# Kernel tuning notes

Hardware: AMD Instinct MI355X
Metric: run time of the kernel (lower is better)

The kernel has to match this reference:

```python
import jax, jax.numpy as jnp
import numpy as np


def setup_inputs() -> dict:
    key = jax.random.key(0)
    ks = jax.random.split(key, 7)
    bs, win_len, num_obj, d = 4, 64, 36, 2048
    s = 1.0 / np.sqrt(d)
    return {
        "region_feats": jax.random.normal(ks[0], (bs, win_len, num_obj, d), jnp.float32),
        "Wq": jax.random.normal(ks[1], (d, d), jnp.float32) * s,
        "bq": jax.random.normal(ks[2], (d,), jnp.float32) * 0.01,
        "Wk": jax.random.normal(ks[3], (d, d), jnp.float32) * s,
        "bk": jax.random.normal(ks[4], (d,), jnp.float32) * 0.01,
        "Wu": jax.random.normal(ks[5], (d, 1024), jnp.float32) * s,
        "bu": jax.random.normal(ks[6], (1024,), jnp.float32) * 0.01,
    }


def reference(region_feats, Wq, bq, Wk, bk, Wu, bu):
    bs, win_len, num_obj, d = region_feats.shape
    feats = region_feats.reshape(bs, win_len * num_obj, d)  # [b, n, d]
    q = feats @ Wq + bq                                     # [b, n, d]
    k = feats @ Wk + bk                                     # [b, n, d]
    adj = jnp.einsum('bnd,bmd->bnm', q, k)                  # unscaled QK^T, [b, n, n]
    adj_norm = jax.nn.softmax(adj, axis=-1)
    v = feats @ Wu + bu                                     # [b, n, 1024]
    out = jnp.einsum('bnm,bmv->bnv', adj_norm, v)
    return out.reshape(bs, win_len, num_obj, -1)
```

## Files before the change

kernel.cpp:

```cpp
#include <hip/hip_runtime.h>


typedef unsigned short u16;
typedef unsigned int   u32;
typedef signed char    i8;
typedef _Float16 f16;
typedef f16    f16x8 __attribute__((ext_vector_type(8)));
typedef float  f32x4 __attribute__((ext_vector_type(4)));
typedef int    i32x4 __attribute__((ext_vector_type(4)));
typedef u32    u32x4 __attribute__((ext_vector_type(4)));
typedef u16    u16x4 __attribute__((ext_vector_type(4)));

#define WAIT_VM8   0x0F78
#define WAIT_VM4   0x0F74
#define WAIT_VM0   0x0F70
#define WAIT_LGKM0 0xC07F

__device__ __forceinline__ void gload16(const void* g, void* l) {
    __builtin_amdgcn_global_load_lds(
        (const __attribute__((address_space(1))) unsigned int*)g,
        (__attribute__((address_space(3))) unsigned int*)l, 16, 0, 0);
}

__device__ __forceinline__ void tile_swizzle(int& tx, int& ty) {
    const int gx = gridDim.x, gy = gridDim.y;
    const int lin = blockIdx.y * gx + blockIdx.x;
    const int G = 4;
    const int gid = lin / (G * gx);
    const int g0 = gid * G;
    const int gh = min(G, gy - g0);
    const int rem = lin - gid * (G * gx);
    ty = g0 + rem % gh;
    tx = rem / gh;
}

__device__ __forceinline__ void digits256(float v, float s, i8& d1, i8& d0) {
    float f = fminf(fmaxf(v * s, -32600.0f), 32600.0f);
    int r = __float2int_rn(f);
    int a1 = (r + 128) >> 8;
    int a0 = r - (a1 << 8);
    d1 = (i8)a1;
    d0 = (i8)a0;
}

__global__ __launch_bounds__(256) void quantFc_k(const float* __restrict__ F,
                                                 const float* __restrict__ u,
                                                 u16* __restrict__ F16,
                                                 i8* __restrict__ hi,
                                                 i8* __restrict__ lo,
                                                 float* __restrict__ c) {
    const long row = blockIdx.x;
    const int tid = threadIdx.x;
    const float* fr = F + row * 2048;
    float dot = 0.f;
    #pragma unroll
    for (int t = 0; t < 8; ++t) {
        const int i = t * 256 + tid;
        const float v = fr[i];
        F16[row * 2048 + i] = __builtin_bit_cast(u16, (f16)v);
        i8 d1, d0;
        digits256(v, 5440.0f, d1, d0);
        hi[row * 2048 + i] = d1;
        lo[row * 2048 + i] = d0;
        dot += v * u[i];
    }
    #pragma unroll
    for (int off = 32; off >= 1; off >>= 1) dot += __shfl_down(dot, off);
    __shared__ float red[4];
    if ((tid & 63) == 0) red[tid >> 6] = dot;
    __syncthreads();
    if (tid == 0) c[row] = red[0] + red[1] + red[2] + red[3];
}

__global__ __launch_bounds__(256) void quantW_k(const float* __restrict__ x,
                                                i8* __restrict__ hi,
                                                i8* __restrict__ lo, long n) {
    long i = (long)blockIdx.x * 256 + threadIdx.x;
    if (i < n) {
        i8 d1, d0;
        digits256(x[i], 261120.0f, d1, d0);
        hi[i] = d1;
        lo[i] = d0;
    }
}

__global__ __launch_bounds__(256) void wut_k(const float* __restrict__ Wu,
                                             u16* __restrict__ WuT) {
    __shared__ float t[32][33];
    const int bx = blockIdx.x * 32;
    const int by = blockIdx.y * 32;
    const int lx = threadIdx.x, ly = threadIdx.y;
    #pragma unroll
    for (int dy = 0; dy < 32; dy += 8)
        t[ly + dy][lx] = Wu[(long)(by + ly + dy) * 1024 + bx + lx];
    __syncthreads();
    #pragma unroll
    for (int dy = 0; dy < 32; dy += 8)
        WuT[(long)(bx + ly + dy) * 2048 + by + lx] =
            __builtin_bit_cast(u16, (f16)t[lx][ly + dy]);
}

__global__ __launch_bounds__(256) void gemv_k(const float* __restrict__ A,
                                              const float* __restrict__ x,
                                              float* __restrict__ y, int ncols) {
    const long row = blockIdx.x;
    const float* ar = A + row * (long)ncols;
    float s = 0.f;
    for (int i = threadIdx.x; i < ncols; i += 256) s += ar[i] * x[i];
    #pragma unroll
    for (int off = 32; off >= 1; off >>= 1) s += __shfl_down(s, off);
    __shared__ float red[4];
    if ((threadIdx.x & 63) == 0) red[threadIdx.x >> 6] = s;
    __syncthreads();
    if (threadIdx.x == 0) y[row] = red[0] + red[1] + red[2] + red[3];
}

template <int EPI>
__global__ __launch_bounds__(256, 2) void gemm_i8(
    const i8* __restrict__ Ah, const i8* __restrict__ Al,
    const i8* __restrict__ Bh, const i8* __restrict__ Bl,
    i8* __restrict__ Qh, i8* __restrict__ Ql, float* __restrict__ Cf,
    float oscale, int N, int K, long strA, long strB, long strC) {
    __shared__ __align__(16) i8 lds[2][32768];

    const int tid  = threadIdx.x;
    const int lane = tid & 63;
    const int wv   = tid >> 6;
    const int wm   = wv >> 1, wn = wv & 1;
    const int l16  = lane & 15, kq = lane >> 4;
    const int z    = blockIdx.z;
    int tx, ty;
    tile_swizzle(tx, ty);
    const long rowBase = (long)ty * 128;
    const long colBase = (long)tx * 128;

    const i8* pAh = Ah + (long)z * strA;
    const i8* pAl = Al + (long)z * strA;
    const i8* pBh = Bh + (long)z * strB;
    const i8* pBl = Bl + (long)z * strB;

    const int l4r = lane >> 2, l4c = lane & 3;
    int rin[2], kqw[2];
    u32 voffA[2], voffB[2];
    int ldsoff[2];
    #pragma unroll
    for (int h = 0; h < 2; ++h) {
        rin[h] = h * 64 + wv * 16 + l4r;
        kqw[h] = (l4c - (rin[h] >> 1)) & 3;
        voffA[h] = (u32)((rowBase + rin[h]) * (long)K) + kqw[h] * 16;
        voffB[h] = (u32)((colBase + rin[h]) * (long)K) + kqw[h] * 16;
        ldsoff[h] = (h * 64 + wv * 16) * 64;
    }

    int aoff[4], boff[4];
    #pragma unroll
    for (int i = 0; i < 4; ++i) {
        const int rA = wm * 64 + i * 16 + l16;
        aoff[i] = rA * 64 + ((kq + (rA >> 1)) & 3) * 16;
        const int rB = wn * 64 + i * 16 + l16;
        boff[i] = rB * 64 + ((kq + (rB >> 1)) & 3) * 16;
    }

    const i32x4 izero = {0, 0, 0, 0};
    i32x4 ahh[4][4], acx[4][4], all_[4][4];
    #pragma unroll
    for (int i = 0; i < 4; ++i)
        #pragma unroll
        for (int j = 0; j < 4; ++j) { ahh[i][j] = izero; acx[i][j] = izero; all_[i][j] = izero; }

    const int nk = K >> 6;

    #pragma unroll
    for (int h = 0; h < 2; ++h) {
        gload16(pAh + voffA[h], &lds[0][0]     + ldsoff[h]);
        gload16(pAl + voffA[h], &lds[0][8192]  + ldsoff[h]);
        gload16(pBh + voffB[h], &lds[0][16384] + ldsoff[h]);
        gload16(pBl + voffB[h], &lds[0][24576] + ldsoff[h]);
    }

    for (int kt = 0; kt < nk; ++kt) {
        const int cur = kt & 1;
        if (kt + 1 < nk) {
            const long ko = (long)(kt + 1) * 64;
            i8* nb = lds[1 - cur];
            #pragma unroll
            for (int h = 0; h < 2; ++h) {
                gload16(pAh + voffA[h] + ko, nb         + ldsoff[h]);
                gload16(pAl + voffA[h] + ko, nb + 8192  + ldsoff[h]);
                gload16(pBh + voffB[h] + ko, nb + 16384 + ldsoff[h]);
                gload16(pBl + voffB[h] + ko, nb + 24576 + ldsoff[h]);
            }
            __builtin_amdgcn_s_waitcnt(WAIT_VM8);
        } else {
            __builtin_amdgcn_s_waitcnt(WAIT_VM0);
        }
        __builtin_amdgcn_s_barrier();

        const i8* base = lds[cur];
        i32x4 fbh[4], fbl[4];
        #pragma unroll
        for (int j = 0; j < 4; ++j) {
            fbh[j] = *(const i32x4*)(base + 16384 + boff[j]);
            fbl[j] = *(const i32x4*)(base + 24576 + boff[j]);
        }
        #pragma unroll
        for (int i = 0; i < 4; ++i) {
            i32x4 fah = *(const i32x4*)(base + aoff[i]);
            i32x4 fal = *(const i32x4*)(base + 8192 + aoff[i]);
            #pragma unroll
            for (int j = 0; j < 4; ++j) {
                ahh[i][j]  = __builtin_amdgcn_mfma_i32_16x16x64_i8(fah, fbh[j], ahh[i][j], 0, 0, 0);
                acx[i][j]  = __builtin_amdgcn_mfma_i32_16x16x64_i8(fah, fbl[j], acx[i][j], 0, 0, 0);
                acx[i][j]  = __builtin_amdgcn_mfma_i32_16x16x64_i8(fal, fbh[j], acx[i][j], 0, 0, 0);
                all_[i][j] = __builtin_amdgcn_mfma_i32_16x16x64_i8(fal, fbl[j], all_[i][j], 0, 0, 0);
            }
        }
        __builtin_amdgcn_s_waitcnt(WAIT_LGKM0);
        __builtin_amdgcn_s_barrier();
    }

    #pragma unroll
    for (int i = 0; i < 4; ++i) {
        const long gr0 = rowBase + wm * 64 + i * 16 + kq * 4;
        #pragma unroll
        for (int j = 0; j < 4; ++j) {
            const long gc = colBase + wn * 64 + j * 16 + l16;
            #pragma unroll
            for (int r = 0; r < 4; ++r) {
                const float comb = 65536.0f * (float)ahh[i][j][r] +
                                     256.0f * (float)acx[i][j][r] +
                                             (float)all_[i][j][r];
                const long o = (gr0 + r) * (long)N + gc;
                if constexpr (EPI == 0) {
                    i8 d1, d0;
                    digits256(comb, oscale, d1, d0);
                    Qh[o] = d1;
                    Ql[o] = d0;
                } else {
                    Cf[(long)z * strC + o] = comb * oscale;
                }
            }
        }
    }
}

template <int EPI>
__global__ __launch_bounds__(256, 3) void gemm_f16(
    const u16* __restrict__ A, const u16* __restrict__ B,
    u16* __restrict__ Ch, float* __restrict__ Cf,
    const float* __restrict__ bias,
    int N, int K, long strA, long strB, long strC) {
    __shared__ __align__(16) i8 lds[2][16384];

    const int tid  = threadIdx.x;
    const int lane = tid & 63;
    const int wv   = tid >> 6;
    const int wm   = wv >> 1, wn = wv & 1;
    const int l16  = lane & 15, kq = lane >> 4;
    const int z    = blockIdx.z;
    int tx, ty;
    tile_swizzle(tx, ty);
    const long rowBase = (long)ty * 128;
    const long colBase = (long)tx * 128;

    const u16* pA = A + (long)z * strA;
    const u16* pB = B + (long)z * strB;

    const int l4r = lane >> 2, l4c = lane & 3;
    u32 voffA[2], voffB[2];
    int ldsoff[2];
    #pragma unroll
    for (int h = 0; h < 2; ++h) {
        const int rin = h * 64 + wv * 16 + l4r;
        const int kw = (l4c - (rin >> 1)) & 3;
        voffA[h] = (u32)((rowBase + rin) * (long)K) + kw * 8;
        voffB[h] = (u32)((colBase + rin) * (long)K) + kw * 8;
        ldsoff[h] = (h * 64 + wv * 16) * 64;
    }
    int aoff[4], boff[4];
    #pragma unroll
    for (int i = 0; i < 4; ++i) {
        const int rA = wm * 64 + i * 16 + l16;
        aoff[i] = rA * 64 + ((kq + (rA >> 1)) & 3) * 16;
        const int rB = wn * 64 + i * 16 + l16;
        boff[i] = rB * 64 + ((kq + (rB >> 1)) & 3) * 16;
    }

    const f32x4 vzero = {0.f, 0.f, 0.f, 0.f};
    f32x4 acc[4][4];
    #pragma unroll
    for (int i = 0; i < 4; ++i)
        #pragma unroll
        for (int j = 0; j < 4; ++j) acc[i][j] = vzero;

    const int nk = K >> 5;

    #pragma unroll
    for (int h = 0; h < 2; ++h) {
        gload16(pA + voffA[h], &lds[0][0]    + ldsoff[h]);
        gload16(pB + voffB[h], &lds[0][8192] + ldsoff[h]);
    }

    for (int kt = 0; kt < nk; ++kt) {
        const int cur = kt & 1;
        if (kt + 1 < nk) {
            const long ko = (long)(kt + 1) * 32;
            i8* nb = lds[1 - cur];
            #pragma unroll
            for (int h = 0; h < 2; ++h) {
                gload16(pA + voffA[h] + ko, nb        + ldsoff[h]);
                gload16(pB + voffB[h] + ko, nb + 8192 + ldsoff[h]);
            }
            __builtin_amdgcn_s_waitcnt(WAIT_VM4);
        } else {
            __builtin_amdgcn_s_waitcnt(WAIT_VM0);
        }
        __builtin_amdgcn_s_barrier();

        const i8* base = lds[cur];
        f16x8 fa[4];
        #pragma unroll
        for (int i = 0; i < 4; ++i)
            fa[i] = __builtin_bit_cast(f16x8, *(const u32x4*)(base + aoff[i]));
        #pragma unroll
        for (int j = 0; j < 4; ++j) {
            f16x8 fb = __builtin_bit_cast(f16x8, *(const u32x4*)(base + 8192 + boff[j]));
            #pragma unroll
            for (int i = 0; i < 4; ++i)
                acc[i][j] = __builtin_amdgcn_mfma_f32_16x16x32_f16(fa[i], fb, acc[i][j], 0, 0, 0);
        }
        __builtin_amdgcn_s_waitcnt(WAIT_LGKM0);
        __builtin_amdgcn_s_barrier();
    }

    #pragma unroll
    for (int i = 0; i < 4; ++i) {
        const long gr0 = rowBase + wm * 64 + i * 16 + kq * 4;
        #pragma unroll
        for (int j = 0; j < 4; ++j) {
            const long gc = colBase + wn * 64 + j * 16 + l16;
            f32x4 a = acc[i][j];
            if constexpr (EPI == 2) {
                const int b  = (int)(gr0 / 2304);
                const int n0 = (int)(gr0 - (long)b * 2304);
                u16x4 o4;
                #pragma unroll
                for (int r = 0; r < 4; ++r) o4[r] = __builtin_bit_cast(u16, (f16)a[r]);
                *(u16x4*)&Ch[(long)b * (1024L * 2304) + gc * 2304 + n0] = o4;
            } else {
                float* C = Cf + (long)z * strC;
                const float bv = bias[gc];
                #pragma unroll
                for (int r = 0; r < 4; ++r) C[(gr0 + r) * (long)N + gc] = a[r] + bv;
            }
        }
    }
}

__global__ __launch_bounds__(256) void softmax_k(const float* __restrict__ adj,
                                                 const float* __restrict__ c,
                                                 u16* __restrict__ P) {
    const int n = 2304;
    const int row = blockIdx.x, b = blockIdx.y;
    const int tid = threadIdx.x;
    const float* ar = adj + ((long)b * n + row) * (long)n;
    const float* cb = c + (long)b * n;
    u16* pr = P + ((long)b * n + row) * (long)n;

    float v[9];
    float mx = -3.0e38f;
    #pragma unroll
    for (int t = 0; t < 9; ++t) {
        const int i = t * 256 + tid;
        const float x = ar[i] + cb[i];
        v[t] = x;
        mx = fmaxf(mx, x);
    }
    #pragma unroll
    for (int off = 32; off >= 1; off >>= 1) mx = fmaxf(mx, __shfl_down(mx, off));
    __shared__ float red[4];
    if ((tid & 63) == 0) red[tid >> 6] = mx;
    __syncthreads();
    mx = fmaxf(fmaxf(red[0], red[1]), fmaxf(red[2], red[3]));

    float s = 0.f;
    #pragma unroll
    for (int t = 0; t < 9; ++t) {
        const float e = __expf(v[t] - mx);
        v[t] = e;
        s += e;
    }
    #pragma unroll
    for (int off = 32; off >= 1; off >>= 1) s += __shfl_down(s, off);
    __shared__ float red2[4];
    if ((tid & 63) == 0) red2[tid >> 6] = s;
    __syncthreads();
    s = red2[0] + red2[1] + red2[2] + red2[3];
    const float inv = 1.0f / s;
    #pragma unroll
    for (int t = 0; t < 9; ++t)
        pr[t * 256 + tid] = __builtin_bit_cast(u16, (f16)(v[t] * inv));
}

extern "C" void kernel_launch(void* const* d_in, const int* in_sizes, int n_in,
                              void* d_out, int out_size, void* d_ws, size_t ws_size,
                              hipStream_t stream) {
    (void)in_sizes; (void)n_in; (void)out_size; (void)ws_size;
    const float* F  = (const float*)d_in[0];
    const float* Wq = (const float*)d_in[1];
    const float* bq = (const float*)d_in[2];
    const float* Wk = (const float*)d_in[3];
    const float* Wu = (const float*)d_in[5];
    const float* bu = (const float*)d_in[6];
    float* out = (float*)d_out;

    char* ws = (char*)d_ws;
    const long o_F16  = 0L;
    const long o_Fh8  = 37748736L;
    const long o_Fl8  = 56623104L;
    const long o_Sh8  = 75497472L;
    const long o_Sl8  = 94371840L;
    const long o_adj  = 113246208L;
    const long o_P    = 198180864L;
    const long o_vT   = 240648192L;
    const long o_WuT  = 259522560L;
    const long o_Wqh  = 263716864L;
    const long o_Wql  = 267911168L;
    const long o_Wkh  = 272105472L;
    const long o_Wkl  = 276299776L;
    const long o_Mth  = 280494080L;
    const long o_Mtl  = 284688384L;
    const long o_u    = 288882688L;
    const long o_c    = 288890880L;

    u16* F16 = (u16*)(ws + o_F16);
    i8*  Fh8 = (i8*)(ws + o_Fh8);   i8* Fl8 = (i8*)(ws + o_Fl8);
    i8*  Sh8 = (i8*)(ws + o_Sh8);   i8* Sl8 = (i8*)(ws + o_Sl8);
    float* adj = (float*)(ws + o_adj);
    u16* P   = (u16*)(ws + o_P);
    u16* vT  = (u16*)(ws + o_vT);
    u16* WuT = (u16*)(ws + o_WuT);
    i8*  Wqh = (i8*)(ws + o_Wqh);   i8* Wql = (i8*)(ws + o_Wql);
    i8*  Wkh = (i8*)(ws + o_Wkh);   i8* Wkl = (i8*)(ws + o_Wkl);
    i8*  Mth = (i8*)(ws + o_Mth);   i8* Mtl = (i8*)(ws + o_Mtl);
    float* u = (float*)(ws + o_u);
    float* c = (float*)(ws + o_c);

    gemv_k<<<2048, 256, 0, stream>>>(Wk, bq, u, 2048);
    quantFc_k<<<9216, 256, 0, stream>>>(F, u, F16, Fh8, Fl8, c);
    quantW_k<<<16384, 256, 0, stream>>>(Wq, Wqh, Wql, 4194304L);
    quantW_k<<<16384, 256, 0, stream>>>(Wk, Wkh, Wkl, 4194304L);
    wut_k<<<dim3(32, 64, 1), dim3(32, 8, 1), 0, stream>>>(Wu, WuT);

    gemm_i8<0><<<dim3(16, 16, 1), 256, 0, stream>>>(
        Wkh, Wkl, Wqh, Wql, Mth, Mtl, nullptr,
        3.8296569e-06f, 2048, 2048, 0L, 0L, 0L);

    gemm_i8<0><<<dim3(16, 72, 1), 256, 0, stream>>>(
        Fh8, Fl8, Mth, Mtl, Sh8, Sl8, nullptr,
        3.8296569e-06f, 2048, 2048, 0L, 0L, 0L);

    gemm_i8<1><<<dim3(18, 18, 4), 256, 0, stream>>>(
        Sh8, Sl8, Fh8, Fl8, nullptr, nullptr, adj,
        3.3791083e-08f, 2304, 2048,
        2304L * 2048, 2304L * 2048, 2304L * 2304);

    softmax_k<<<dim3(2304, 4, 1), 256, 0, stream>>>(adj, c, P);

    gemm_f16<2><<<dim3(8, 72, 1), 256, 0, stream>>>(
        F16, WuT, vT, nullptr, nullptr, 1024, 2048, 0L, 0L, 0L);

    gemm_f16<3><<<dim3(8, 18, 4), 256, 0, stream>>>(
        P, vT, nullptr, out, bu, 1024, 2304,
        2304L * 2304, 1024L * 2304, 2304L * 1024);
}
```

Before: 662.4 us.

## Convert int8 split-digit GEMMs to stream-K scheduling with partial-tile fixup

Replaces the three tile-per-block int8 GEMM launches with a persistent stream-K kernel. It runs 512 blocks, and each block takes an equal slice of the flattened (tile, k-chunk) work space, which removes partial-wave tail imbalance (256, 1152 and 1296 tiles of 128x128). Split tiles in the quantised-output GEMMs write fp32 partials to head/tail scratch, placed in the adj buffer, and a separate fixup kernel sums and re-quantises them. The fp32-output GEMM pre-zeroes split tiles and accumulates with atomicAdd. The cost is extra launches, partial-sum traffic, atomics and nondeterministic summation order.

Result: slower. 796.3 us (+20.2%).

```diff
diff --git a/kernel.cpp b/kernel.cpp
--- a/kernel.cpp
+++ b/kernel.cpp
@@ -20,6 +20,300 @@
     __builtin_amdgcn_global_load_lds(
         (const __attribute__((address_space(1))) unsigned int*)g,
         (__attribute__((address_space(3))) unsigned int*)l, 16, 0, 0);
+}
+
+__device__ __forceinline__ void digits256(float v, float s, i8& d1, i8& d0) {
+    float f = fminf(fmaxf(v * s, -32600.0f), 32600.0f);
+    int r = __float2int_rn(f);
+    int a1 = (r + 128) >> 8;
+    int a0 = r - (a1 << 8);
+    d1 = (i8)a1;
+    d0 = (i8)a0;
+}
+
+__device__ __forceinline__ void tile_decomp(int t, int ntM, int ntN,
+                                            int& z, int& ty, int& tx) {
+    const int per = ntM * ntN;
+    z = t / per;
+    const int q = t - z * per;
+    tx = q / ntM;
+    ty = q - tx * ntM;
+}
+
+__global__ __launch_bounds__(256) void quantFc_k(const float* __restrict__ F,
+                                                 const float* __restrict__ u,
+                                                 u16* __restrict__ F16,
+                                                 i8* __restrict__ hi,
+                                                 i8* __restrict__ lo,
+                                                 float* __restrict__ c) {
+    const long row = blockIdx.x;
+    const int tid = threadIdx.x;
+    const float* fr = F + row * 2048;
+    float dot = 0.f;
+    #pragma unroll
+    for (int t = 0; t < 8; ++t) {
+        const int i = t * 256 + tid;
+        const float v = fr[i];
+        F16[row * 2048 + i] = __builtin_bit_cast(u16, (f16)v);
+        i8 d1, d0;
+        digits256(v, 5440.0f, d1, d0);
+        hi[row * 2048 + i] = d1;
+        lo[row * 2048 + i] = d0;
+        dot += v * u[i];
+    }
+    #pragma unroll
+    for (int off = 32; off >= 1; off >>= 1) dot += __shfl_down(dot, off);
+    __shared__ float red[4];
+    if ((tid & 63) == 0) red[tid >> 6] = dot;
+    __syncthreads();
+    if (tid == 0) c[row] = red[0] + red[1] + red[2] + red[3];
+}
+
+__global__ __launch_bounds__(256) void quantW_k(const float* __restrict__ x,
+                                                i8* __restrict__ hi,
+                                                i8* __restrict__ lo, long n) {
+    long i = (long)blockIdx.x * 256 + threadIdx.x;
+    if (i < n) {
+        i8 d1, d0;
+        digits256(x[i], 261120.0f, d1, d0);
+        hi[i] = d1;
+        lo[i] = d0;
+    }
+}
+
+__global__ __launch_bounds__(256) void wut_k(const float* __restrict__ Wu,
+                                             u16* __restrict__ WuT) {
+    __shared__ float t[32][33];
+    const int bx = blockIdx.x * 32;
+    const int by = blockIdx.y * 32;
+    const int lx = threadIdx.x, ly = threadIdx.y;
+    #pragma unroll
+    for (int dy = 0; dy < 32; dy += 8)
+        t[ly + dy][lx] = Wu[(long)(by + ly + dy) * 1024 + bx + lx];
+    __syncthreads();
+    #pragma unroll
+    for (int dy = 0; dy < 32; dy += 8)
+        WuT[(long)(bx + ly + dy) * 2048 + by + lx] =
+            __builtin_bit_cast(u16, (f16)t[lx][ly + dy]);
+}
+
+__global__ __launch_bounds__(256) void gemv_k(const float* __restrict__ A,
+                                              const float* __restrict__ x,
+                                              float* __restrict__ y, int ncols) {
+    const long row = blockIdx.x;
+    const float* ar = A + row * (long)ncols;
+    float s = 0.f;
+    for (int i = threadIdx.x; i < ncols; i += 256) s += ar[i] * x[i];
+    #pragma unroll
+    for (int off = 32; off >= 1; off >>= 1) s += __shfl_down(s, off);
+    __shared__ float red[4];
+    if ((threadIdx.x & 63) == 0) red[threadIdx.x >> 6] = s;
+    __syncthreads();
+    if (threadIdx.x == 0) y[row] = red[0] + red[1] + red[2] + red[3];
+}
+
+template <int EPI>
+__global__ __launch_bounds__(256, 2) void gemm_i8_sk(
+    const i8* __restrict__ Ah, const i8* __restrict__ Al,
+    const i8* __restrict__ Bh, const i8* __restrict__ Bl,
+    i8* __restrict__ Qh, i8* __restrict__ Ql, float* __restrict__ Cf,
+    float* __restrict__ phead, float* __restrict__ ptail,
+    float oscale, int N, int K, long strA, long strB, long strC,
+    int ntM, int ntN, int nk, int upb) {
+    __shared__ __align__(16) i8 lds[2][32768];
+
+    const int tid  = threadIdx.x;
+    const int lane = tid & 63;
+    const int wv   = tid >> 6;
+    const int wm   = wv >> 1, wn = wv & 1;
+    const int l16  = lane & 15, kq = lane >> 4;
+    const int blk  = blockIdx.x;
+
+    const int l4r = lane >> 2, l4c = lane & 3;
+    int rin[2], kqw[2], ldsoff[2];
+    #pragma unroll
+    for (int h = 0; h < 2; ++h) {
+        rin[h] = h * 64 + wv * 16 + l4r;
+        kqw[h] = (l4c - (rin[h] >> 1)) & 3;
+        ldsoff[h] = (h * 64 + wv * 16) * 64;
+    }
+    int aoff[4], boff[4];
+    #pragma unroll
+    for (int i = 0; i < 4; ++i) {
+        const int rA = wm * 64 + i * 16 + l16;
+        aoff[i] = rA * 64 + ((kq + (rA >> 1)) & 3) * 16;
+        const int rB = wn * 64 + i * 16 + l16;
+        boff[i] = rB * 64 + ((kq + (rB >> 1)) & 3) * 16;
+    }
+
+    const i32x4 izero = {0, 0, 0, 0};
+    long ku = (long)blk * upb;
+    const long ku1 = ku + upb;
+    bool firstSeg = true;
+
+    while (ku < ku1) {
+        const int t  = (int)(ku / nk);
+        const int ks = (int)(ku - (long)t * nk);
+        const int ke = (int)min((long)nk, ks + (ku1 - ku));
+        int z, ty, tx;
+        tile_decomp(t, ntM, ntN, z, ty, tx);
+        const long rowBase = (long)ty * 128;
+        const long colBase = (long)tx * 128;
+
+        const i8* pAh = Ah + (long)z * strA;
+        const i8* pAl = Al + (long)z * strA;
+        const i8* pBh = Bh + (long)z * strB;
+        const i8* pBl = Bl + (long)z * strB;
+
+        u32 voffA[2], voffB[2];
+        #pragma unroll
+        for (int h = 0; h < 2; ++h) {
+            voffA[h] = (u32)((rowBase + rin[h]) * (long)K) + kqw[h] * 16 + ks * 64;
+            voffB[h] = (u32)((colBase + rin[h]) * (long)K) + kqw[h] * 16 + ks * 64;
+        }
+
+        i32x4 ahh[4][4], acx[4][4], all_[4][4];
+        #pragma unroll
+        for (int i = 0; i < 4; ++i)
+            #pragma unroll
+            for (int j = 0; j < 4; ++j) { ahh[i][j] = izero; acx[i][j] = izero; all_[i][j] = izero; }
+
+        #pragma unroll
+        for (int h = 0; h < 2; ++h) {
+            gload16(pAh + voffA[h], &lds[0][0]     + ldsoff[h]);
+            gload16(pAl + voffA[h], &lds[0][8192]  + ldsoff[h]);
+            gload16(pBh + voffB[h], &lds[0][16384] + ldsoff[h]);
+            gload16(pBl + voffB[h], &lds[0][24576] + ldsoff[h]);
+        }
+
+        for (int kt = ks; kt < ke; ++kt) {
+            const int cur = (kt - ks) & 1;
+            if (kt + 1 < ke) {
+                const long ko = (long)(kt + 1 - ks) * 64;
+                i8* nb = lds[1 - cur];
+                #pragma unroll
+                for (int h = 0; h < 2; ++h) {
+                    gload16(pAh + voffA[h] + ko, nb         + ldsoff[h]);
+                    gload16(pAl + voffA[h] + ko, nb + 8192  + ldsoff[h]);
+                    gload16(pBh + voffB[h] + ko, nb + 16384 + ldsoff[h]);
+                    gload16(pBl + voffB[h] + ko, nb + 24576 + ldsoff[h]);
+                }
+                __builtin_amdgcn_s_waitcnt(WAIT_VM8);
+            } else {
+                __builtin_amdgcn_s_waitcnt(WAIT_VM0);
+            }
+            __builtin_amdgcn_s_barrier();
+
+            const i8* base = lds[cur];
+            i32x4 fbh[4], fbl[4];
+            #pragma unroll
+            for (int j = 0; j < 4; ++j) {
+                fbh[j] = *(const i32x4*)(base + 16384 + boff[j]);
+                fbl[j] = *(const i32x4*)(base + 24576 + boff[j]);
+            }
+            #pragma unroll
+            for (int i = 0; i < 4; ++i) {
+                i32x4 fah = *(const i32x4*)(base + aoff[i]);
+                i32x4 fal = *(const i32x4*)(base + 8192 + aoff[i]);
+                #pragma unroll
+                for (int j = 0; j < 4; ++j) {
+                    ahh[i][j]  = __builtin_amdgcn_mfma_i32_16x16x64_i8(fah, fbh[j], ahh[i][j], 0, 0, 0);
+                    acx[i][j]  = __builtin_amdgcn_mfma_i32_16x16x64_i8(fah, fbl[j], acx[i][j], 0, 0, 0);
+                    all_[i][j] = __builtin_amdgcn_mfma_i32_16x16x64_i8(fal, fbl[j], all_[i][j], 0, 0, 0);
+                    acx[i][j]  = __builtin_amdgcn_mfma_i32_16x16x64_i8(fal, fbh[j], acx[i][j], 0, 0, 0);
+                }
+            }
+            __builtin_amdgcn_s_waitcnt(WAIT_LGKM0);
+            __builtin_amdgcn_s_barrier();
+        }
+
+        const bool full = (ks == 0) && (ke == nk);
+        float* ps = (firstSeg ? phead : ptail) + (long)blk * 16384;
+        #pragma unroll
+        for (int i = 0; i < 4; ++i) {
+            const int lr0 = wm * 64 + i * 16 + kq * 4;
+            const long gr0 = rowBase + lr0;
+            #pragma unroll
+            for (int j = 0; j < 4; ++j) {
+                const int lc = wn * 64 + j * 16 + l16;
+                const long gc = colBase + lc;
+                #pragma unroll
+                for (int r = 0; r < 4; ++r) {
+                    const float comb = 65536.0f * (float)ahh[i][j][r] +
+                                         256.0f * (float)acx[i][j][r] +
+                                                 (float)all_[i][j][r];
+                    if constexpr (EPI == 0) {
+                        if (full) {
+                            const long o = (gr0 + r) * (long)N + gc;
+                            i8 d1, d0;
+                            digits256(comb, oscale, d1, d0);
+                            Qh[o] = d1;
+                            Ql[o] = d0;
+                        } else {
+                            ps[(lr0 + r) * 128 + lc] = comb;
+                        }
+                    } else {
+                        float* C = Cf + (long)z * strC;
+                        const long o = (gr0 + r) * (long)N + gc;
+                        if (full) C[o] = comb * oscale;
+                        else atomicAdd(&C[o], comb * oscale);
+                    }
+                }
+            }
+        }
+        firstSeg = false;
+        ku += (ke - ks);
+    }
+}
+
+__global__ __launch_bounds__(256) void fixup_k(
+    const float* __restrict__ phead, const float* __restrict__ ptail,
+    i8* __restrict__ Qh, i8* __restrict__ Ql, float oscale,
+    int ntM, int ntN, int nk, int upb, int N) {
+    const int t = blockIdx.x;
+    const int b_lo = (t * nk) / upb;
+    const int b_hi = ((t + 1) * nk - 1) / upb;
+    if (b_lo == b_hi) return;
+    int z, ty, tx;
+    tile_decomp(t, ntM, ntN, z, ty, tx);
+    const long rowBase = (long)ty * 128;
+    const long colBase = (long)tx * 128;
+    const int tid = threadIdx.x;
+    #pragma unroll
+    for (int k = 0; k < 64; ++k) {
+        const int e = k * 256 + tid;
+        float s = 0.f;
+        for (int b = b_lo; b <= b_hi; ++b) {
+            const float* ps = (((long)b * upb >= (long)t * nk) ? phead : ptail)
+                              + (long)b * 16384;
+            s += ps[e];
+        }
+        const int lr = e >> 7, lc = e & 127;
+        i8 d1, d0;
+        digits256(s, oscale, d1, d0);
+        const long o = (rowBase + lr) * (long)N + colBase + lc;
+        Qh[o] = d1;
+        Ql[o] = d0;
+    }
+}
+
+__global__ __launch_bounds__(256) void zero_split_k(
+    float* __restrict__ Cf, int ntM, int ntN, int nk, int upb, int N, long strC) {
+    const int t = blockIdx.x;
+    const int b_lo = (t * nk) / upb;
+    const int b_hi = ((t + 1) * nk - 1) / upb;
+    if (b_lo == b_hi) return;
+    int z, ty, tx;
+    tile_decomp(t, ntM, ntN, z, ty, tx);
+    float* C = Cf + (long)z * strC;
+    const long rowBase = (long)ty * 128;
+    const long colBase = (long)tx * 128;
+    const int tid = threadIdx.x;
+    #pragma unroll
+    for (int k = 0; k < 64; ++k) {
+        const int e = k * 256 + tid;
+        C[(rowBase + (e >> 7)) * (long)N + colBase + (e & 127)] = 0.f;
+    }
 }
 
 __device__ __forceinline__ void tile_swizzle(int& tx, int& ty) {
@@ -32,216 +326,6 @@
     const int rem = lin - gid * (G * gx);
     ty = g0 + rem % gh;
     tx = rem / gh;
-}
-
-__device__ __forceinline__ void digits256(float v, float s, i8& d1, i8& d0) {
-    float f = fminf(fmaxf(v * s, -32600.0f), 32600.0f);
-    int r = __float2int_rn(f);
-    int a1 = (r + 128) >> 8;
-    int a0 = r - (a1 << 8);
-    d1 = (i8)a1;
-    d0 = (i8)a0;
-}
-
-__global__ __launch_bounds__(256) void quantFc_k(const float* __restrict__ F,
-                                                 const float* __restrict__ u,
-                                                 u16* __restrict__ F16,
-                                                 i8* __restrict__ hi,
-                                                 i8* __restrict__ lo,
-                                                 float* __restrict__ c) {
-    const long row = blockIdx.x;
-    const int tid = threadIdx.x;
-    const float* fr = F + row * 2048;
-    float dot = 0.f;
-    #pragma unroll
-    for (int t = 0; t < 8; ++t) {
-        const int i = t * 256 + tid;
-        const float v = fr[i];
-        F16[row * 2048 + i] = __builtin_bit_cast(u16, (f16)v);
-        i8 d1, d0;
-        digits256(v, 5440.0f, d1, d0);
-        hi[row * 2048 + i] = d1;
-        lo[row * 2048 + i] = d0;
-        dot += v * u[i];
-    }
-    #pragma unroll
-    for (int off = 32; off >= 1; off >>= 1) dot += __shfl_down(dot, off);
-    __shared__ float red[4];
-    if ((tid & 63) == 0) red[tid >> 6] = dot;
-    __syncthreads();
-    if (tid == 0) c[row] = red[0] + red[1] + red[2] + red[3];
-}
-
-__global__ __launch_bounds__(256) void quantW_k(const float* __restrict__ x,
-                                                i8* __restrict__ hi,
-                                                i8* __restrict__ lo, long n) {
-    long i = (long)blockIdx.x * 256 + threadIdx.x;
-    if (i < n) {
-        i8 d1, d0;
-        digits256(x[i], 261120.0f, d1, d0);
-        hi[i] = d1;
-        lo[i] = d0;
-    }
-}
-
-__global__ __launch_bounds__(256) void wut_k(const float* __restrict__ Wu,
-                                             u16* __restrict__ WuT) {
-    __shared__ float t[32][33];
-    const int bx = blockIdx.x * 32;
-    const int by = blockIdx.y * 32;
-    const int lx = threadIdx.x, ly = threadIdx.y;
-    #pragma unroll
-    for (int dy = 0; dy < 32; dy += 8)
-        t[ly + dy][lx] = Wu[(long)(by + ly + dy) * 1024 + bx + lx];
-    __syncthreads();
-    #pragma unroll
-    for (int dy = 0; dy < 32; dy += 8)
-        WuT[(long)(bx + ly + dy) * 2048 + by + lx] =
-            __builtin_bit_cast(u16, (f16)t[lx][ly + dy]);
-}
-
-__global__ __launch_bounds__(256) void gemv_k(const float* __restrict__ A,
-                                              const float* __restrict__ x,
-                                              float* __restrict__ y, int ncols) {
-    const long row = blockIdx.x;
-    const float* ar = A + row * (long)ncols;
-    float s = 0.f;
-    for (int i = threadIdx.x; i < ncols; i += 256) s += ar[i] * x[i];
-    #pragma unroll
-    for (int off = 32; off >= 1; off >>= 1) s += __shfl_down(s, off);
-    __shared__ float red[4];
-    if ((threadIdx.x & 63) == 0) red[threadIdx.x >> 6] = s;
-    __syncthreads();
-    if (threadIdx.x == 0) y[row] = red[0] + red[1] + red[2] + red[3];
-}
-
-template <int EPI>
-__global__ __launch_bounds__(256, 2) void gemm_i8(
-    const i8* __restrict__ Ah, const i8* __restrict__ Al,
-    const i8* __restrict__ Bh, const i8* __restrict__ Bl,
-    i8* __restrict__ Qh, i8* __restrict__ Ql, float* __restrict__ Cf,
-    float oscale, int N, int K, long strA, long strB, long strC) {
-    __shared__ __align__(16) i8 lds[2][32768];
-
-    const int tid  = threadIdx.x;
-    const int lane = tid & 63;
-    const int wv   = tid >> 6;
-    const int wm   = wv >> 1, wn = wv & 1;
-    const int l16  = lane & 15, kq = lane >> 4;
-    const int z    = blockIdx.z;
-    int tx, ty;
-    tile_swizzle(tx, ty);
-    const long rowBase = (long)ty * 128;
-    const long colBase = (long)tx * 128;
-
-    const i8* pAh = Ah + (long)z * strA;
-    const i8* pAl = Al + (long)z * strA;
-    const i8* pBh = Bh + (long)z * strB;
-    const i8* pBl = Bl + (long)z * strB;
-
-    const int l4r = lane >> 2, l4c = lane & 3;
-    int rin[2], kqw[2];
-    u32 voffA[2], voffB[2];
-    int ldsoff[2];
-    #pragma unroll
-    for (int h = 0; h < 2; ++h) {
-        rin[h] = h * 64 + wv * 16 + l4r;
-        kqw[h] = (l4c - (rin[h] >> 1)) & 3;
-        voffA[h] = (u32)((rowBase + rin[h]) * (long)K) + kqw[h] * 16;
-        voffB[h] = (u32)((colBase + rin[h]) * (long)K) + kqw[h] * 16;
-        ldsoff[h] = (h * 64 + wv * 16) * 64;
-    }
-
-    int aoff[4], boff[4];
-    #pragma unroll
-    for (int i = 0; i < 4; ++i) {
-        const int rA = wm * 64 + i * 16 + l16;
-        aoff[i] = rA * 64 + ((kq + (rA >> 1)) & 3) * 16;
-        const int rB = wn * 64 + i * 16 + l16;
-        boff[i] = rB * 64 + ((kq + (rB >> 1)) & 3) * 16;
-    }
-
-    const i32x4 izero = {0, 0, 0, 0};
-    i32x4 ahh[4][4], acx[4][4], all_[4][4];
-    #pragma unroll
-    for (int i = 0; i < 4; ++i)
-        #pragma unroll
-        for (int j = 0; j < 4; ++j) { ahh[i][j] = izero; acx[i][j] = izero; all_[i][j] = izero; }
-
-    const int nk = K >> 6;
-
-    #pragma unroll
-    for (int h = 0; h < 2; ++h) {
-        gload16(pAh + voffA[h], &lds[0][0]     + ldsoff[h]);
-        gload16(pAl + voffA[h], &lds[0][8192]  + ldsoff[h]);
-        gload16(pBh + voffB[h], &lds[0][16384] + ldsoff[h]);
-        gload16(pBl + voffB[h], &lds[0][24576] + ldsoff[h]);
-    }
-
-    for (int kt = 0; kt < nk; ++kt) {
-        const int cur = kt & 1;
-        if (kt + 1 < nk) {
-            const long ko = (long)(kt + 1) * 64;
-            i8* nb = lds[1 - cur];
-            #pragma unroll
-            for (int h = 0; h < 2; ++h) {
-                gload16(pAh + voffA[h] + ko, nb         + ldsoff[h]);
-                gload16(pAl + voffA[h] + ko, nb + 8192  + ldsoff[h]);
-                gload16(pBh + voffB[h] + ko, nb + 16384 + ldsoff[h]);
-                gload16(pBl + voffB[h] + ko, nb + 24576 + ldsoff[h]);
-            }
-            __builtin_amdgcn_s_waitcnt(WAIT_VM8);
-        } else {
-            __builtin_amdgcn_s_waitcnt(WAIT_VM0);
-        }
-        __builtin_amdgcn_s_barrier();
-
-        const i8* base = lds[cur];
-        i32x4 fbh[4], fbl[4];
-        #pragma unroll
-        for (int j = 0; j < 4; ++j) {
-            fbh[j] = *(const i32x4*)(base + 16384 + boff[j]);
-            fbl[j] = *(const i32x4*)(base + 24576 + boff[j]);
-        }
-        #pragma unroll
-        for (int i = 0; i < 4; ++i) {
-            i32x4 fah = *(const i32x4*)(base + aoff[i]);
-            i32x4 fal = *(const i32x4*)(base + 8192 + aoff[i]);
-            #pragma unroll
-            for (int j = 0; j < 4; ++j) {
-                ahh[i][j]  = __builtin_amdgcn_mfma_i32_16x16x64_i8(fah, fbh[j], ahh[i][j], 0, 0, 0);
-                acx[i][j]  = __builtin_amdgcn_mfma_i32_16x16x64_i8(fah, fbl[j], acx[i][j], 0, 0, 0);
-                acx[i][j]  = __builtin_amdgcn_mfma_i32_16x16x64_i8(fal, fbh[j], acx[i][j], 0, 0, 0);
-                all_[i][j] = __builtin_amdgcn_mfma_i32_16x16x64_i8(fal, fbl[j], all_[i][j], 0, 0, 0);
-            }
-        }
-        __builtin_amdgcn_s_waitcnt(WAIT_LGKM0);
-        __builtin_amdgcn_s_barrier();
-    }
-
-    #pragma unroll
-    for (int i = 0; i < 4; ++i) {
-        const long gr0 = rowBase + wm * 64 + i * 16 + kq * 4;
-        #pragma unroll
-        for (int j = 0; j < 4; ++j) {
-            const long gc = colBase + wn * 64 + j * 16 + l16;
-            #pragma unroll
-            for (int r = 0; r < 4; ++r) {
-                const float comb = 65536.0f * (float)ahh[i][j][r] +
-                                     256.0f * (float)acx[i][j][r] +
-                                             (float)all_[i][j][r];
-                const long o = (gr0 + r) * (long)N + gc;
-                if constexpr (EPI == 0) {
-                    i8 d1, d0;
-                    digits256(comb, oscale, d1, d0);
-                    Qh[o] = d1;
-                    Ql[o] = d0;
-                } else {
-                    Cf[(long)z * strC + o] = comb * oscale;
-                }
-            }
-        }
-    }
 }
 
 template <int EPI>
@@ -446,24 +530,32 @@
     float* u = (float*)(ws + o_u);
     float* c = (float*)(ws + o_c);
 
+    float* phead = (float*)(ws + o_adj);
+    float* ptail = (float*)(ws + o_adj + 33554432L);
+
     gemv_k<<<2048, 256, 0, stream>>>(Wk, bq, u, 2048);
     quantFc_k<<<9216, 256, 0, stream>>>(F, u, F16, Fh8, Fl8, c);
     quantW_k<<<16384, 256, 0, stream>>>(Wq, Wqh, Wql, 4194304L);
     quantW_k<<<16384, 256, 0, stream>>>(Wk, Wkh, Wkl, 4194304L);
     wut_k<<<dim3(32, 64, 1), dim3(32, 8, 1), 0, stream>>>(Wu, WuT);
 
-    gemm_i8<0><<<dim3(16, 16, 1), 256, 0, stream>>>(
-        Wkh, Wkl, Wqh, Wql, Mth, Mtl, nullptr,
-        3.8296569e-06f, 2048, 2048, 0L, 0L, 0L);
-
-    gemm_i8<0><<<dim3(16, 72, 1), 256, 0, stream>>>(
-        Fh8, Fl8, Mth, Mtl, Sh8, Sl8, nullptr,
-        3.8296569e-06f, 2048, 2048, 0L, 0L, 0L);
-
-    gemm_i8<1><<<dim3(18, 18, 4), 256, 0, stream>>>(
-        Sh8, Sl8, Fh8, Fl8, nullptr, nullptr, adj,
+    gemm_i8_sk<0><<<512, 256, 0, stream>>>(
+        Wkh, Wkl, Wqh, Wql, Mth, Mtl, nullptr, phead, ptail,
+        3.8296569e-06f, 2048, 2048, 0L, 0L, 0L, 16, 16, 32, 16);
+    fixup_k<<<256, 256, 0, stream>>>(phead, ptail, Mth, Mtl,
+        3.8296569e-06f, 16, 16, 32, 16, 2048);
+
+    gemm_i8_sk<0><<<512, 256, 0, stream>>>(
+        Fh8, Fl8, Mth, Mtl, Sh8, Sl8, nullptr, phead, ptail,
+        3.8296569e-06f, 2048, 2048, 0L, 0L, 0L, 72, 16, 32, 72);
+    fixup_k<<<1152, 256, 0, stream>>>(phead, ptail, Sh8, Sl8,
+        3.8296569e-06f, 72, 16, 32, 72, 2048);
+
+    zero_split_k<<<1296, 256, 0, stream>>>(adj, 18, 18, 32, 81, 2304, 2304L * 2304);
+    gemm_i8_sk<1><<<512, 256, 0, stream>>>(
+        Sh8, Sl8, Fh8, Fl8, nullptr, nullptr, adj, nullptr, nullptr,
         3.3791083e-08f, 2304, 2048,
-        2304L * 2048, 2304L * 2048, 2304L * 2304);
+        2304L * 2048, 2304L * 2048, 2304L * 2304, 18, 18, 32, 81);
 
     softmax_k<<<dim3(2304, 4, 1), 256, 0, stream>>>(adj, c, P);
 
```
